# Kernel tuning notes

Measured on AMD Instinct MI355X. Metric: run time of the kernel, lower is better.

Reference implementation:

```python
import jax, jax.numpy as jnp
import numpy as np

B, T, C, H = 2, 2048, 1024, 16
HD = C // H
EPS = 1e-5


def setup_inputs() -> dict:
    key = jax.random.key(0)
    ks = jax.random.split(key, 16)
    s = 0.02
    return {
        "x": jax.random.normal(ks[0], (B, T, C), jnp.float32),
        "ln1_w": jnp.ones((C,), jnp.float32),
        "ln1_b": jnp.zeros((C,), jnp.float32),
        "ln2_w": jnp.ones((C,), jnp.float32),
        "ln2_b": jnp.zeros((C,), jnp.float32),
        "Wq": jax.random.normal(ks[1], (C, C), jnp.float32) * s,
        "bq": jnp.zeros((C,), jnp.float32),
        "Wk": jax.random.normal(ks[2], (C, C), jnp.float32) * s,
        "bk": jnp.zeros((C,), jnp.float32),
        "Wv": jax.random.normal(ks[3], (C, C), jnp.float32) * s,
        "bv": jnp.zeros((C,), jnp.float32),
        "Wp": jax.random.normal(ks[4], (C, C), jnp.float32) * s,
        "bp": jnp.zeros((C,), jnp.float32),
        "W1": jax.random.normal(ks[5], (4 * C, C), jnp.float32) * s,
        "b1": jnp.zeros((4 * C,), jnp.float32),
        "W2": jax.random.normal(ks[6], (C, 4 * C), jnp.float32) * s,
        "b2": jnp.zeros((C,), jnp.float32),
    }


def _ln(x, w, b):
    mu = jnp.mean(x, axis=-1, keepdims=True)
    var = jnp.mean((x - mu) ** 2, axis=-1, keepdims=True)
    return (x - mu) * jax.lax.rsqrt(var + EPS) * w + b


def _heads(t):  # (B,T,C) -> (B,H,T,HD)
    return t.reshape(B, T, H, HD).transpose(0, 2, 1, 3)


def reference(x, ln1_w, ln1_b, ln2_w, ln2_b, Wq, bq, Wk, bk, Wv, bv, Wp, bp, W1, b1, W2, b2):
    h = _ln(x, ln1_w, ln1_b)
    q = _heads(h @ Wq.T + bq)
    k = _heads(h @ Wk.T + bk)
    v = _heads(h @ Wv.T + bv)
    att = jnp.einsum("bhqd,bhkd->bhqk", q, k) * (1.0 / np.sqrt(HD))
    causal = jnp.tril(jnp.ones((T, T), bool))
    att = jnp.where(causal, att, -jnp.inf)
    att = jax.nn.softmax(att, axis=-1)
    y = jnp.einsum("bhqk,bhkd->bhqd", att, v)
    y = y.transpose(0, 2, 1, 3).reshape(B, T, C)
    x = x + (y @ Wp.T + bp)
    h2 = _ln(x, ln2_w, ln2_b)
    m = jax.nn.gelu(h2 @ W1.T + b1, approximate=False)
    x = x + (m @ W2.T + b2)
    return x
```

## Files before the change

kernel.cpp:

```cpp
#include <hip/hip_runtime.h>

#define TB 2
#define TT 2048
#define TC 1024
#define TH 16
#define THD 64
#define LNEPS 1e-5f

typedef _Float16 f16;
typedef __attribute__((ext_vector_type(8))) _Float16 f16x8;
typedef __attribute__((ext_vector_type(4))) _Float16 f16x4;
typedef __attribute__((ext_vector_type(4))) float f32x4;

__device__ __forceinline__ f32x4 mfma_16x16x32(f16x8 a, f16x8 b, f32x4 c) {
    return __builtin_amdgcn_mfma_f32_16x16x32_f16(a, b, c, 0, 0, 0);
}

__device__ __forceinline__ void load_lds16(const f16* g, f16* l) {
    __builtin_amdgcn_global_load_lds(
        (const __attribute__((address_space(1))) unsigned int*)g,
        (__attribute__((address_space(3))) unsigned int*)l, 16, 0, 0);
}

__device__ __forceinline__ float gelu_fast(float v) {
    float u = 0.7978845608f * v * (1.f + 0.044715f * v * v);
    float e = __expf(2.f * u);
    return v - v / (e + 1.f);
}

__global__ __launch_bounds__(256) void ln_kernel(const float* __restrict__ x,
                                                 const float* __restrict__ w,
                                                 const float* __restrict__ bsrc,
                                                 f16* __restrict__ out) {
    int row  = blockIdx.x * 4 + (threadIdx.x >> 6);
    int lane = threadIdx.x & 63;
    const float4* xr = (const float4*)(x + (size_t)row * TC);
    float4 v[4];
    float s = 0.f, ss = 0.f;
#pragma unroll
    for (int i = 0; i < 4; i++) {
        v[i] = xr[i * 64 + lane];
        s  += v[i].x + v[i].y + v[i].z + v[i].w;
        ss += v[i].x * v[i].x + v[i].y * v[i].y + v[i].z * v[i].z + v[i].w * v[i].w;
    }
#pragma unroll
    for (int off = 32; off > 0; off >>= 1) {
        s  += __shfl_xor(s, off);
        ss += __shfl_xor(ss, off);
    }
    float mean = s * (1.f / TC);
    float var  = ss * (1.f / TC) - mean * mean;
    float rstd = rsqrtf(var + LNEPS);
    const float4* wv = (const float4*)w;
    const float4* bv = (const float4*)bsrc;
    f16x4* ov = (f16x4*)(out + (size_t)row * TC);
#pragma unroll
    for (int i = 0; i < 4; i++) {
        int idx = i * 64 + lane;
        float4 wc = wv[idx], bc = bv[idx];
        f16x4 o;
        o[0] = (f16)((v[i].x - mean) * rstd * wc.x + bc.x);
        o[1] = (f16)((v[i].y - mean) * rstd * wc.y + bc.y);
        o[2] = (f16)((v[i].z - mean) * rstd * wc.z + bc.z);
        o[3] = (f16)((v[i].w - mean) * rstd * wc.w + bc.w);
        ov[idx] = o;
    }
}

__global__ void cvt_all_kernel(const float* __restrict__ Wq, const float* __restrict__ Wk,
                               const float* __restrict__ Wv, const float* __restrict__ Wp,
                               const float* __restrict__ W1, const float* __restrict__ W2,
                               f16* __restrict__ dst) {
    int i = blockIdx.x * blockDim.x + threadIdx.x;
    const int Q = 262144;
    const float* src;
    int j;
    int s = i >> 18;
    if (s < 4) {
        src = (s == 0) ? Wq : (s == 1) ? Wk : (s == 2) ? Wv : Wp;
        j = i & (Q - 1);
    } else if (s < 8) {
        src = W1; j = i - 4 * Q;
    } else {
        src = W2; j = i - 8 * Q;
    }
    float4 v = ((const float4*)src)[j];
    f16x4 o;
    o[0] = (f16)v.x; o[1] = (f16)v.y; o[2] = (f16)v.z; o[3] = (f16)v.w;
    ((f16x4*)dst)[i] = o;
}

template <int BM, int BN, int BK, int EPI>
__global__ __launch_bounds__(256) void gemm_kernel(const f16* __restrict__ A,
                                                   const f16* __restrict__ W,
                                                   const float* __restrict__ bias,
                                                   const float* __restrict__ bias2,
                                                   const float* __restrict__ bias3,
                                                   const float* __restrict__ res,
                                                   void* __restrict__ outp,
                                                   int M, int N, int K) {
    constexpr int CPR = BK / 8;
    __shared__ __align__(16) f16 sA[BM * BK];
    __shared__ __align__(16) f16 sB[BN * BK];
    const int t  = threadIdx.x;
    const int m0 = blockIdx.y * BM;
    const int n0 = blockIdx.x * BN;
    const int wid = t >> 6, lane = t & 63;
    const int wr = wid >> 1, wc = wid & 1;
    constexpr int WM = BM / 2, WN = BN / 2;
    constexpr int MI = WM / 16, NI = WN / 16;
    f32x4 acc[MI][NI];
#pragma unroll
    for (int i = 0; i < MI; i++)
#pragma unroll
        for (int j = 0; j < NI; j++) acc[i][j] = (f32x4){0.f, 0.f, 0.f, 0.f};
    const int quad = lane >> 4, l15 = lane & 15;

    for (int k0 = 0; k0 < K; k0 += BK) {
#pragma unroll
        for (int i = 0; i < BM * CPR / 256; i++) {
            int p = t + i * 256;
            int row = p / CPR, pc = p % CPR;
            int c = (pc - (row >> 1)) & (CPR - 1);
            load_lds16(&A[(size_t)(m0 + row) * K + k0 + c * 8], &sA[p * 8]);
        }
#pragma unroll
        for (int i = 0; i < BN * CPR / 256; i++) {
            int p = t + i * 256;
            int row = p / CPR, pc = p % CPR;
            int c = (pc - (row >> 1)) & (CPR - 1);
            load_lds16(&W[(size_t)(n0 + row) * K + k0 + c * 8], &sB[p * 8]);
        }
        __syncthreads();
#pragma unroll
        for (int ks = 0; ks < BK / 32; ks++) {
            f16x8 af[MI], bf[NI];
#pragma unroll
            for (int i = 0; i < MI; i++) {
                int r = wr * WM + i * 16 + l15;
                af[i] = *(const f16x8*)&sA[(r * CPR + ((ks * 4 + quad + (r >> 1)) & (CPR - 1))) * 8];
            }
#pragma unroll
            for (int j = 0; j < NI; j++) {
                int r = wc * WN + j * 16 + l15;
                bf[j] = *(const f16x8*)&sB[(r * CPR + ((ks * 4 + quad + (r >> 1)) & (CPR - 1))) * 8];
            }
#pragma unroll
            for (int i = 0; i < MI; i++)
#pragma unroll
                for (int j = 0; j < NI; j++)
                    acc[i][j] = mfma_16x16x32(af[i], bf[j], acc[i][j]);
        }
        __syncthreads();
    }

#pragma unroll
    for (int i = 0; i < MI; i++) {
#pragma unroll
        for (int j = 0; j < NI; j++) {
            int col   = n0 + wc * WN + j * 16 + l15;
            int rbase = m0 + wr * WM + i * 16 + quad * 4;
            float bvv = bias ? bias[col] : 0.f;
#pragma unroll
            for (int r = 0; r < 4; r++) {
                size_t idx = (size_t)(rbase + r) * N + col;
                float v = acc[i][j][r] + bvv;
                if constexpr (EPI == 1) {
                    ((float*)outp)[idx] = v + res[idx];
                } else {
                    ((f16*)outp)[idx] = (f16)v;
                }
            }
        }
    }
}

#define BARF() do { __builtin_amdgcn_s_barrier(); asm volatile("" ::: "memory"); } while (0)

template <int EPI>
__global__ __launch_bounds__(512, 2) void gemm256_kernel(
    const f16* __restrict__ A, const f16* __restrict__ W,
    const float* __restrict__ bias, const float* __restrict__ bias2,
    const float* __restrict__ bias3,
    f16* __restrict__ out0, f16* __restrict__ out1,
    f16* __restrict__ out2, f16* __restrict__ out3,
    int M, int N, int K) {
    __shared__ __align__(16) f16 lds[8 * 8192];
    f16* sA = lds;
    f16* sB = lds + 4 * 8192;
    const int t    = threadIdx.x;
    const int lane = t & 63, wid = t >> 6;
    const int quad = lane >> 4, l15 = lane & 15;
    const int wr = wid >> 2, wc = wid & 3;
    const int m0 = blockIdx.y * 256, n0 = blockIdx.x * 256;
    int kbeg = 0, nsub = K >> 5;
    f16* outp = out0;
    if constexpr (EPI == 4) {
        int Kc = K >> 2;
        kbeg = blockIdx.z * Kc;
        nsub = Kc >> 5;
        outp = (blockIdx.z == 0) ? out0 : (blockIdx.z == 1) ? out1
             : (blockIdx.z == 2) ? out2 : out3;
    }
    const f16* Abase = A + (size_t)m0 * K + kbeg;
    const f16* Wbase = W + (size_t)n0 * K + kbeg;

    int srow[2], sgo[2], sld[2];
#pragma unroll
    for (int i = 0; i < 2; i++) {
        int p = t + i * 512;
        int r = p >> 2;
        srow[i] = r;
        sgo[i]  = (((p & 3) - (r >> 1)) & 3) * 8;
        sld[i]  = p * 8;
    }
    auto stageA = [&](int s) {
        if (s >= nsub) return;
        f16* dst = sA + (s & 3) * 8192;
        const f16* src = Abase + s * 32;
#pragma unroll
        for (int i = 0; i < 2; i++)
            load_lds16(src + (size_t)srow[i] * K + sgo[i], dst + sld[i]);
    };
    auto stageB = [&](int s) {
        if (s >= nsub) return;
        f16* dst = sB + (s & 3) * 8192;
        const f16* src = Wbase + s * 32;
#pragma unroll
        for (int i = 0; i < 2; i++)
            load_lds16(src + (size_t)srow[i] * K + sgo[i], dst + sld[i]);
    };

    int offA[8], offB[4];
#pragma unroll
    for (int q = 0; q < 8; q++) {
        int row = wr * 128 + q * 16 + l15;
        offA[q] = row * 32 + (((quad + (row >> 1)) & 3) * 8);
    }
#pragma unroll
    for (int q = 0; q < 4; q++) {
        int row = wc * 64 + q * 16 + l15;
        offB[q] = row * 32 + (((quad + (row >> 1)) & 3) * 8);
    }

    f32x4 acc[8][4];
#pragma unroll
    for (int i = 0; i < 8; i++)
#pragma unroll
        for (int j = 0; j < 4; j++) acc[i][j] = (f32x4){0.f, 0.f, 0.f, 0.f};

    stageA(0); stageB(0); stageA(1); stageB(1); stageA(2); stageB(2);
    asm volatile("s_waitcnt vmcnt(8)" ::: "memory");
    BARF();

    for (int s = 0; s < nsub; s += 2) {
#pragma unroll
        for (int h = 0; h < 2; h++) {
            const int su = s + h;
            const f16* slA = sA + (su & 3) * 8192;
            const f16* slB = sB + (su & 3) * 8192;
            f16x8 af[4], bf[4];
#pragma unroll
            for (int q = 0; q < 4; q++) af[q] = *(const f16x8*)&slA[offA[q]];
#pragma unroll
            for (int q = 0; q < 4; q++) bf[q] = *(const f16x8*)&slB[offB[q]];
            stageA(su + 3);
            __builtin_amdgcn_s_barrier();
            asm volatile("s_waitcnt lgkmcnt(0)" ::: "memory");
            __builtin_amdgcn_s_setprio(1);
#pragma unroll
            for (int i = 0; i < 4; i++)
#pragma unroll
                for (int j = 0; j < 4; j++)
                    acc[i][j] = mfma_16x16x32(af[i], bf[j], acc[i][j]);
            __builtin_amdgcn_s_setprio(0);
            asm volatile("" ::: "memory");
            BARF();
#pragma unroll
            for (int q = 0; q < 4; q++) af[q] = *(const f16x8*)&slA[offA[4 + q]];
            stageB(su + 3);
            __builtin_amdgcn_s_barrier();
            asm volatile("s_waitcnt lgkmcnt(0)" ::: "memory");
            __builtin_amdgcn_s_setprio(1);
#pragma unroll
            for (int i = 0; i < 4; i++)
#pragma unroll
                for (int j = 0; j < 4; j++)
                    acc[4 + i][j] = mfma_16x16x32(af[i], bf[j], acc[4 + i][j]);
            __builtin_amdgcn_s_setprio(0);
            if (su + 3 < nsub)      asm volatile("s_waitcnt vmcnt(8)" ::: "memory");
            else if (su + 2 < nsub) asm volatile("s_waitcnt vmcnt(4)" ::: "memory");
            else                    asm volatile("s_waitcnt vmcnt(0)" ::: "memory");
            BARF();
        }
    }

#pragma unroll
    for (int fr = 0; fr < 8; fr++) {
#pragma unroll
        for (int fc = 0; fc < 4; fc++) {
            int col   = n0 + wc * 64 + fc * 16 + l15;
            int rbase = m0 + wr * 128 + fr * 16 + quad * 4;
            float bvv = 0.f;
            if constexpr (EPI == 3)
                bvv = (col < 1024) ? bias[col]
                    : (col < 2048) ? bias2[col - 1024] : bias3[col - 2048];
            else if constexpr (EPI == 2)
                bvv = bias[col];
#pragma unroll
            for (int r = 0; r < 4; r++) {
                size_t idx = (size_t)(rbase + r) * N + col;
                float v = acc[fr][fc][r] + bvv;
                if constexpr (EPI == 2) outp[idx] = (f16)gelu_fast(v);
                else                    outp[idx] = (f16)v;
            }
        }
    }
}

__global__ __launch_bounds__(256) void reduce4_kernel(const f16* __restrict__ p0,
                                                      const f16* __restrict__ p1,
                                                      const f16* __restrict__ p2,
                                                      const f16* __restrict__ p3,
                                                      const float* __restrict__ b2,
                                                      float* __restrict__ x1) {
    int i = blockIdx.x * 256 + threadIdx.x;
    f16x4 a = ((const f16x4*)p0)[i], b = ((const f16x4*)p1)[i];
    f16x4 c = ((const f16x4*)p2)[i], d = ((const f16x4*)p3)[i];
    float4 r = ((float4*)x1)[i];
    float4 bb = ((const float4*)b2)[i & 255];
    r.x += (float)a[0] + (float)b[0] + (float)c[0] + (float)d[0] + bb.x;
    r.y += (float)a[1] + (float)b[1] + (float)c[1] + (float)d[1] + bb.y;
    r.z += (float)a[2] + (float)b[2] + (float)c[2] + (float)d[2] + bb.z;
    r.w += (float)a[3] + (float)b[3] + (float)c[3] + (float)d[3] + bb.w;
    ((float4*)x1)[i] = r;
}

__global__ __launch_bounds__(256) void transpose_kernel(const f16* __restrict__ in,
                                                        f16* __restrict__ out) {
    __shared__ f16 tile[32][33];
    int bt = blockIdx.x;
    int b  = bt / (TT / 32);
    int t0 = (bt % (TT / 32)) * 32;
    int c0 = blockIdx.y * 32;
    int tx = threadIdx.x & 31;
    int ty = threadIdx.x >> 5;
    for (int r = ty; r < 32; r += 8)
        tile[r][tx] = in[(size_t)(b * TT + t0 + r) * 3072 + 2048 + c0 + tx];
    __syncthreads();
    for (int r = ty; r < 32; r += 8)
        out[(size_t)(b * TC + c0 + r) * TT + t0 + tx] = tile[tx][r];
}

__global__ __launch_bounds__(256, 4) void attn_kernel(const f16* __restrict__ qkv,
                                                      const f16* __restrict__ vtg,
                                                      f16* __restrict__ yg) {
    __shared__ __align__(16) f16 sK[2][64 * 64];
    __shared__ __align__(16) f16 sV[2][64 * 64];
    __shared__ __align__(16) f16 pl[4][16 * 64];
    const int t    = threadIdx.x;
    const int wid  = t >> 6, lane = t & 63;
    const int quad = lane >> 4, l15 = lane & 15;
    const int idx = blockIdx.x;
    const int u = idx & 255, r = idx >> 8;
    const int bh = u & 31, rc = u >> 5;
    const int qblk = (r == 0) ? rc : (r == 1) ? 31 - rc : (r == 2) ? 8 + rc : 23 - rc;
    const int b = bh >> 4, h = bh & 15;
    const int q0 = qblk * 64;
    const int q0w = q0 + wid * 16;

    const f16* qptr = qkv + (size_t)(b * TT) * 3072 + h * THD;
    const f16* kptr = qptr + 1024;

    f16x8 qa0, qa1;
    {
        const f16* qb_ = qptr + (size_t)(q0w + l15) * 3072 + quad * 8;
        qa0 = *(const f16x8*)qb_;
        qa1 = *(const f16x8*)(qb_ + 32);
#pragma unroll
        for (int j = 0; j < 8; j++) { qa0[j] *= (f16)0.125f; qa1[j] *= (f16)0.125f; }
    }

    auto stage = [&](int buf, int k0) {
#pragma unroll
        for (int i = 0; i < 2; i++) {
            int p = t + i * 256;
            int row = p >> 3, c0 = p & 7;
            int cc = c0 ^ (row & 7);
            load_lds16(kptr + (size_t)(k0 + row) * 3072 + cc * 8, &sK[buf][p * 8]);
            load_lds16(vtg + (size_t)(bh * THD + row) * TT + k0 + cc * 8, &sV[buf][p * 8]);
        }
    };

    f32x4 o[4];
#pragma unroll
    for (int j = 0; j < 4; j++) o[j] = (f32x4){0.f, 0.f, 0.f, 0.f};
    float mcol = -__builtin_inff(), lsum = 0.f;
    f16* plw = pl[wid];
    const int sw = (l15 & 7) << 1;
    const int nt = qblk + 1;

    stage(0, 0);
    for (int it = 0; it < nt; it++) {
        const int cur = it & 1;
        __syncthreads();
        if (it + 1 < nt) stage(cur ^ 1, (it + 1) * 64);
        const int k0 = it * 64;
        if (k0 <= q0w + 15) {
            const f16* sk = sK[cur];
            f32x4 s[4];
#pragma unroll
            for (int g = 0; g < 4; g++) {
                int key = g * 16 + l15;
                f16x8 klo = *(const f16x8*)&sk[(key * 8 + (quad ^ (l15 & 7))) * 8];
                f16x8 khi = *(const f16x8*)&sk[(key * 8 + ((quad + 4) ^ (l15 & 7))) * 8];
                f32x4 a = (f32x4){0.f, 0.f, 0.f, 0.f};
                a = mfma_16x16x32(klo, qa0, a);
                a = mfma_16x16x32(khi, qa1, a);
                s[g] = a;
            }
            const bool full = (k0 + 63 <= q0w);
            float lm = -__builtin_inff();
#pragma unroll
            for (int g = 0; g < 4; g++) {
#pragma unroll
                for (int rr = 0; rr < 4; rr++) {
                    if (!full) {
                        int key = k0 + g * 16 + quad * 4 + rr;
                        if (key > q0w + l15) s[g][rr] = -__builtin_inff();
                    }
                    lm = fmaxf(lm, s[g][rr]);
                }
            }
            lm = fmaxf(lm, __shfl_xor(lm, 16));
            lm = fmaxf(lm, __shfl_xor(lm, 32));
            float mnew  = fmaxf(mcol, lm);
            float alpha = __expf(mcol - mnew);
            mcol = mnew;
            float sum = 0.f;
#pragma unroll
            for (int g = 0; g < 4; g++) {
                f16x4 pw;
#pragma unroll
                for (int rr = 0; rr < 4; rr++) {
                    float p = __expf(s[g][rr] - mnew);
                    sum += p;
                    pw[rr] = (f16)p;
                }
                *(f16x4*)&plw[(l15 * 16 + ((g * 4 + quad) ^ sw)) * 4] = pw;
            }
            sum += __shfl_xor(sum, 16);
            sum += __shfl_xor(sum, 32);
            lsum = lsum * alpha + sum;
#pragma unroll
            for (int j = 0; j < 4; j++) {
                o[j][0] *= alpha; o[j][1] *= alpha; o[j][2] *= alpha; o[j][3] *= alpha;
            }
            __asm__ volatile("s_waitcnt lgkmcnt(0)" ::: "memory");
            const f16* sv = sV[cur];
#pragma unroll
            for (int hh = 0; hh < 2; hh++) {
                f16x8 pb = *(const f16x8*)&plw[(l15 * 16 + ((hh * 8 + quad * 2) ^ sw)) * 4];
#pragma unroll
                for (int j = 0; j < 4; j++) {
                    int d = j * 16 + l15;
                    f16x8 vf = *(const f16x8*)&sv[(d * 8 + ((4 * hh + quad) ^ (l15 & 7))) * 8];
                    o[j] = mfma_16x16x32(vf, pb, o[j]);
                }
            }
        }
    }
    float inv = 1.f / lsum;
    size_t rowbase = (size_t)(b * TT + q0w + l15) * TC + h * THD;
#pragma unroll
    for (int j = 0; j < 4; j++) {
        f16x4 ov;
#pragma unroll
        for (int rr = 0; rr < 4; rr++) ov[rr] = (f16)(o[j][rr] * inv);
        *(f16x4*)&yg[rowbase + j * 16 + quad * 4] = ov;
    }
}

extern "C" void kernel_launch(void* const* d_in, const int* in_sizes, int n_in,
                              void* d_out, int out_size, void* d_ws, size_t ws_size,
                              hipStream_t stream) {
    const float* x    = (const float*)d_in[0];
    const float* ln1w = (const float*)d_in[1];
    const float* ln1b = (const float*)d_in[2];
    const float* ln2w = (const float*)d_in[3];
    const float* ln2b = (const float*)d_in[4];
    const float* Wq   = (const float*)d_in[5];
    const float* bq   = (const float*)d_in[6];
    const float* Wk   = (const float*)d_in[7];
    const float* bk   = (const float*)d_in[8];
    const float* Wv   = (const float*)d_in[9];
    const float* bv   = (const float*)d_in[10];
    const float* Wp   = (const float*)d_in[11];
    const float* bp   = (const float*)d_in[12];
    const float* W1   = (const float*)d_in[13];
    const float* b1   = (const float*)d_in[14];
    const float* W2   = (const float*)d_in[15];
    const float* b2   = (const float*)d_in[16];

    char* ws = (char*)d_ws;
    const size_t MB = 1024 * 1024;
    f16* hb   = (f16*)(ws + 0);
    f16* qkv  = (f16*)(ws + 8 * MB);
    f16* vT   = (f16*)(ws + 32 * MB);
    f16* mb   = (f16*)(ws + 16 * MB);
    f16* Wb   = (f16*)(ws + 48 * MB);
    f16* Wqb  = Wb;
    f16* Wpb  = Wb + (size_t)3 * 1024 * 1024;
    f16* W1b  = Wb + (size_t)4 * 1024 * 1024;
    f16* W2b  = Wb + (size_t)8 * 1024 * 1024;
    f16* yb   = hb;
    f16* h2b  = qkv;
    f16* part0 = (f16*)(ws + 0);
    f16* part1 = (f16*)(ws + 8 * MB);
    f16* part2 = (f16*)(ws + 48 * MB);
    f16* part3 = (f16*)(ws + 56 * MB);
    float* x1 = (float*)d_out;

    cvt_all_kernel<<<12288, 256, 0, stream>>>(Wq, Wk, Wv, Wp, W1, W2, Wb);
    ln_kernel<<<1024, 256, 0, stream>>>(x, ln1w, ln1b, hb);

    gemm256_kernel<3><<<dim3(3072 / 256, (TB * TT) / 256), 512, 0, stream>>>(
        hb, Wqb, bq, bk, bv, qkv, nullptr, nullptr, nullptr, TB * TT, 3072, TC);
    transpose_kernel<<<dim3(TB * TT / 32, TC / 32), 256, 0, stream>>>(qkv, vT);
    attn_kernel<<<1024, 256, 0, stream>>>(qkv, vT, yb);
    gemm_kernel<128, 64, 64, 1><<<dim3(TC / 64, (TB * TT) / 128), 256, 0, stream>>>(
        yb, Wpb, bp, nullptr, nullptr, x, x1, TB * TT, TC, TC);
    ln_kernel<<<1024, 256, 0, stream>>>(x1, ln2w, ln2b, h2b);
    gemm256_kernel<2><<<dim3(4 * TC / 256, (TB * TT) / 256), 512, 0, stream>>>(
        h2b, W1b, b1, nullptr, nullptr, mb, nullptr, nullptr, nullptr, TB * TT, 4 * TC, TC);
    gemm256_kernel<4><<<dim3(TC / 256, (TB * TT) / 256, 4), 512, 0, stream>>>(
        mb, W2b, nullptr, nullptr, nullptr, part0, part1, part2, part3, TB * TT, TC, 4 * TC);
    reduce4_kernel<<<4096, 256, 0, stream>>>(part0, part1, part2, part3, b2, x1);
}
```

Before: 344.5 us.

## Fuse weight conversion with first layernorm; split attention into two launches

Weight fp32->fp16 conversion and the first LayerNorm now run in one kernel, with extra blocks for the LN rows, which saves one launch. The attention launch is also split into two launches of 512 blocks, each covering half the query blocks with a new interleaved ordering meant to balance causal work. The split adds a launch and a tail at each launch boundary, and it changes how work is spread across CUs.

```diff
diff --git a/kernel.cpp b/kernel.cpp
--- a/kernel.cpp
+++ b/kernel.cpp
@@ -67,27 +67,67 @@
     }
 }
 
-__global__ void cvt_all_kernel(const float* __restrict__ Wq, const float* __restrict__ Wk,
-                               const float* __restrict__ Wv, const float* __restrict__ Wp,
-                               const float* __restrict__ W1, const float* __restrict__ W2,
-                               f16* __restrict__ dst) {
-    int i = blockIdx.x * blockDim.x + threadIdx.x;
-    const int Q = 262144;
-    const float* src;
-    int j;
-    int s = i >> 18;
-    if (s < 4) {
-        src = (s == 0) ? Wq : (s == 1) ? Wk : (s == 2) ? Wv : Wp;
-        j = i & (Q - 1);
-    } else if (s < 8) {
-        src = W1; j = i - 4 * Q;
+__global__ __launch_bounds__(256) void prep_kernel(
+    const float* __restrict__ Wq, const float* __restrict__ Wk,
+    const float* __restrict__ Wv, const float* __restrict__ Wp,
+    const float* __restrict__ W1, const float* __restrict__ W2,
+    f16* __restrict__ dst,
+    const float* __restrict__ x, const float* __restrict__ lnw,
+    const float* __restrict__ lnb, f16* __restrict__ out) {
+    int bid = blockIdx.x;
+    if (bid < 12288) {
+        int i = bid * 256 + threadIdx.x;
+        const int Q = 262144;
+        const float* src;
+        int j;
+        int s = i >> 18;
+        if (s < 4) {
+            src = (s == 0) ? Wq : (s == 1) ? Wk : (s == 2) ? Wv : Wp;
+            j = i & (Q - 1);
+        } else if (s < 8) {
+            src = W1; j = i - 4 * Q;
+        } else {
+            src = W2; j = i - 8 * Q;
+        }
+        float4 v = ((const float4*)src)[j];
+        f16x4 o;
+        o[0] = (f16)v.x; o[1] = (f16)v.y; o[2] = (f16)v.z; o[3] = (f16)v.w;
+        ((f16x4*)dst)[i] = o;
     } else {
-        src = W2; j = i - 8 * Q;
-    }
-    float4 v = ((const float4*)src)[j];
-    f16x4 o;
-    o[0] = (f16)v.x; o[1] = (f16)v.y; o[2] = (f16)v.z; o[3] = (f16)v.w;
-    ((f16x4*)dst)[i] = o;
+        int row  = (bid - 12288) * 4 + (threadIdx.x >> 6);
+        int lane = threadIdx.x & 63;
+        const float4* xr = (const float4*)(x + (size_t)row * TC);
+        float4 v[4];
+        float s = 0.f, ss = 0.f;
+#pragma unroll
+        for (int i = 0; i < 4; i++) {
+            v[i] = xr[i * 64 + lane];
+            s  += v[i].x + v[i].y + v[i].z + v[i].w;
+            ss += v[i].x * v[i].x + v[i].y * v[i].y + v[i].z * v[i].z + v[i].w * v[i].w;
+        }
+#pragma unroll
+        for (int off = 32; off > 0; off >>= 1) {
+            s  += __shfl_xor(s, off);
+            ss += __shfl_xor(ss, off);
+        }
+        float mean = s * (1.f / TC);
+        float var  = ss * (1.f / TC) - mean * mean;
+        float rstd = rsqrtf(var + LNEPS);
+        const float4* wv = (const float4*)lnw;
+        const float4* bv = (const float4*)lnb;
+        f16x4* ov = (f16x4*)(out + (size_t)row * TC);
+#pragma unroll
+        for (int i = 0; i < 4; i++) {
+            int idx = i * 64 + lane;
+            float4 wc = wv[idx], bc = bv[idx];
+            f16x4 o;
+            o[0] = (f16)((v[i].x - mean) * rstd * wc.x + bc.x);
+            o[1] = (f16)((v[i].y - mean) * rstd * wc.y + bc.y);
+            o[2] = (f16)((v[i].z - mean) * rstd * wc.z + bc.z);
+            o[3] = (f16)((v[i].w - mean) * rstd * wc.w + bc.w);
+            ov[idx] = o;
+        }
+    }
 }
 
 template <int BM, int BN, int BK, int EPI>
@@ -354,7 +394,8 @@
 
 __global__ __launch_bounds__(256, 4) void attn_kernel(const f16* __restrict__ qkv,
                                                       const f16* __restrict__ vtg,
-                                                      f16* __restrict__ yg) {
+                                                      f16* __restrict__ yg,
+                                                      int qbase) {
     __shared__ __align__(16) f16 sK[2][64 * 64];
     __shared__ __align__(16) f16 sV[2][64 * 64];
     __shared__ __align__(16) f16 pl[4][16 * 64];
@@ -362,9 +403,9 @@
     const int wid  = t >> 6, lane = t & 63;
     const int quad = lane >> 4, l15 = lane & 15;
     const int idx = blockIdx.x;
-    const int u = idx & 255, r = idx >> 8;
-    const int bh = u & 31, rc = u >> 5;
-    const int qblk = (r == 0) ? rc : (r == 1) ? 31 - rc : (r == 2) ? 8 + rc : 23 - rc;
+    const int bh = idx & 31;
+    const int qi = idx >> 5;
+    const int qblk = qbase + ((qi < 8) ? qi : 23 - qi);
     const int b = bh >> 4, h = bh & 15;
     const int q0 = qblk * 64;
     const int q0w = q0 + wid * 16;
@@ -521,13 +562,14 @@
     f16* part3 = (f16*)(ws + 56 * MB);
     float* x1 = (float*)d_out;
 
-    cvt_all_kernel<<<12288, 256, 0, stream>>>(Wq, Wk, Wv, Wp, W1, W2, Wb);
-    ln_kernel<<<1024, 256, 0, stream>>>(x, ln1w, ln1b, hb);
+    prep_kernel<<<13312, 256, 0, stream>>>(Wq, Wk, Wv, Wp, W1, W2, Wb,
+                                           x, ln1w, ln1b, hb);
 
     gemm256_kernel<3><<<dim3(3072 / 256, (TB * TT) / 256), 512, 0, stream>>>(
         hb, Wqb, bq, bk, bv, qkv, nullptr, nullptr, nullptr, TB * TT, 3072, TC);
     transpose_kernel<<<dim3(TB * TT / 32, TC / 32), 256, 0, stream>>>(qkv, vT);
-    attn_kernel<<<1024, 256, 0, stream>>>(qkv, vT, yb);
+    attn_kernel<<<512, 256, 0, stream>>>(qkv, vT, yb, 0);
+    attn_kernel<<<512, 256, 0, stream>>>(qkv, vT, yb, 16);
     gemm_kernel<128, 64, 64, 1><<<dim3(TC / 64, (TB * TT) / 128), 256, 0, stream>>>(
         yb, Wpb, bp, nullptr, nullptr, x, x1, TB * TT, TC, TC);
     ln_kernel<<<1024, 256, 0, stream>>>(x1, ln2w, ln2b, h2b);
```

New measurement: 366.3 us. 1.06x slower.
